# Performance work log

Hardware: AMD Instinct MI355X
Metric: run time of the kernel (lower is better)

The kernel has to match this reference:

```python
import jax, jax.numpy as jnp
import numpy as np

B, S, HID = 2, 2048, 2048
H, KVH, D = 32, 8, 64
G = H // KVH  # kv groups


def _rotate_half(x):
    x1, x2 = jnp.split(x, 2, axis=-1)
    return jnp.concatenate((-x2, x1), axis=-1)


def setup_inputs() -> dict:
    key = jax.random.key(0)
    ks = jax.random.split(key, 7)
    return {
        "hidden_states": jax.random.normal(ks[0], (B, S, HID), dtype=jnp.float32),
        "cos": jax.random.normal(ks[1], (B, S, D), dtype=jnp.float32),
        "sin": jax.random.normal(ks[2], (B, S, D), dtype=jnp.float32),
        "attention_mask": jnp.ones((B, S), dtype=bool),
        "Wq": jax.random.normal(ks[3], (HID, HID), dtype=jnp.float32) * 0.02,
        "Wk": jax.random.normal(ks[4], (KVH * D, HID), dtype=jnp.float32) * 0.02,
        "Wv": jax.random.normal(ks[5], (KVH * D, HID), dtype=jnp.float32) * 0.02,
        "Wo": jax.random.normal(ks[6], (HID, HID), dtype=jnp.float32) * 0.02,
    }


def reference(hidden_states, cos, sin, attention_mask, Wq, Wk, Wv, Wo):
    scaling = D ** (-0.5)
    # projections -> [B, heads, S, D]
    q = jnp.einsum('bsh,eh->bse', hidden_states, Wq).reshape(B, S, H, D).transpose(0, 2, 1, 3)
    k = jnp.einsum('bsh,eh->bse', hidden_states, Wk).reshape(B, S, KVH, D).transpose(0, 2, 1, 3)
    v = jnp.einsum('bsh,eh->bse', hidden_states, Wv).reshape(B, S, KVH, D).transpose(0, 2, 1, 3)
    # RoPE (cos/sin broadcast over head dim 1)
    c = cos[:, None, :, :]
    s = sin[:, None, :, :]
    q = q * c + _rotate_half(q) * s
    k = k * c + _rotate_half(k) * s
    # GQA: view q as [B, KVH, G, S, D]; avoid materializing expanded k/v
    qg = q.reshape(B, KVH, G, S, D)
    scores = jnp.einsum('bkgsd,bktd->bkgst', qg, k) * scaling  # [B,KVH,G,S,T]
    mask = attention_mask[:, None, None, None, :]  # [B,1,1,1,T]
    scores = jnp.where(mask, scores, -jnp.inf)
    attn = jax.nn.softmax(scores, axis=-1)
    out = jnp.einsum('bkgst,bktd->bkgsd', attn, v)  # [B,KVH,G,S,D]
    out = out.reshape(B, H, S, D).transpose(0, 2, 1, 3).reshape(B, S, H * D)
    return jnp.einsum('bse,he->bsh', out, Wo)
```

## Files before the change

kernel.cpp:

```cpp
#include <hip/hip_runtime.h>


typedef __attribute__((ext_vector_type(8))) short bf16x8;
typedef __attribute__((ext_vector_type(4))) float f32x4;

#define MFMA_BF16(a, b, c) __builtin_amdgcn_mfma_f32_16x16x32_bf16((a), (b), (c), 0, 0, 0)

#define QSCALE 0.1803368801111204f

static __device__ __forceinline__ unsigned short f2b(float f) {
  unsigned int u = __float_as_uint(f);
  return (unsigned short)((u + 0x7FFFu + ((u >> 16) & 1u)) >> 16);
}

typedef __attribute__((address_space(1))) void gvoid;
typedef __attribute__((address_space(3))) void svoid;
static __device__ __forceinline__ void gll16(const void* g, void* l) {
  __builtin_amdgcn_global_load_lds((gvoid*)g, (svoid*)l, 16, 0, 0);
}

typedef __attribute__((address_space(3))) unsigned short lds_us;
static __device__ __forceinline__ unsigned lof(unsigned short* p) {
  return (unsigned)(unsigned long long)(lds_us*)p;
}

template <int OFF>
static __device__ __forceinline__ bf16x8 dsr(unsigned a) {
  bf16x8 r;
  asm volatile("ds_read_b128 %0, %1 offset:%2" : "=v"(r) : "v"(a), "i"(OFF));
  return r;
}

template <int N>
static __device__ __forceinline__ void vm() {
  if constexpr (N >= 0) asm volatile("s_waitcnt vmcnt(%0)" ::"i"(N) : "memory");
}

#define BARRIER() asm volatile("s_barrier" ::: "memory")
#define LGKM0()                                        \
  do {                                                 \
    asm volatile("s_waitcnt lgkmcnt(0)" ::: "memory"); \
    __builtin_amdgcn_sched_barrier(0);                 \
  } while (0)

__global__ __launch_bounds__(256) void cvt4(
    const float* __restrict__ s0, const float* __restrict__ s1,
    const float* __restrict__ s2, const float* __restrict__ s3,
    unsigned short* __restrict__ d0, unsigned short* __restrict__ d1,
    unsigned short* __restrict__ d2, unsigned short* __restrict__ d3) {
  int i = blockIdx.x * 256 + threadIdx.x;
  const float* s; unsigned short* d; int off;
  if (i < 2097152)      { s = s0; d = d0; off = i; }
  else if (i < 3145728) { s = s1; d = d1; off = i - 2097152; }
  else if (i < 3407872) { s = s2; d = d2; off = i - 3145728; }
  else                  { s = s3; d = d3; off = i - 3407872; }
  float4 f = ((const float4*)s)[off];
  ushort4 o;
  o.x = f2b(f.x); o.y = f2b(f.y); o.z = f2b(f.z); o.w = f2b(f.w);
  ((ushort4*)d)[off] = o;
}

__global__ __launch_bounds__(256) void cvt_f32_bf16(const float* __restrict__ src,
                                                    unsigned short* __restrict__ dst,
                                                    int n4) {
  int i = blockIdx.x * 256 + threadIdx.x;
  if (i < n4) {
    float4 f = ((const float4*)src)[i];
    ushort4 o;
    o.x = f2b(f.x); o.y = f2b(f.y); o.z = f2b(f.z); o.w = f2b(f.w);
    ((ushort4*)dst)[i] = o;
  }
}


__global__ __launch_bounds__(512, 2) void gemm_qkv(
    const unsigned short* __restrict__ X,
    const unsigned short* __restrict__ W,
    const float* __restrict__ cosp,
    const float* __restrict__ sinp,
    unsigned short* __restrict__ Qo,
    unsigned short* __restrict__ Ko,
    unsigned short* __restrict__ Vto) {
  constexpr int K = 2048;
  __shared__ unsigned short As[2][16384];
  __shared__ unsigned short Bs[2][12288];

  const int tid = threadIdx.x;
  const int lane = tid & 63;
  const int w = tid >> 6;
  const int lane15 = lane & 15, quad = lane >> 4;
  const int l7 = lane15 & 7;

  const int id = blockIdx.x;
  const int wg = (id & 7) * 32 + (id >> 3);
  const int m0 = (wg >> 4) * 256;
  const int n0 = (wg & 15) * 192;

  f32x4 acc[2][12];
#pragma unroll
  for (int i = 0; i < 2; ++i)
#pragma unroll
    for (int j = 0; j < 12; ++j) acc[i][j] = (f32x4){0.f, 0.f, 0.f, 0.f};

  const int rl8 = lane >> 3;
  const int sc8 = ((lane & 7) ^ rl8) * 8;
  const unsigned short* Ab = X + (size_t)(m0 + w * 8 + rl8) * K + sc8;
  const unsigned short* Bb = W + (size_t)(n0 + w * 8 + rl8) * K + sc8;

  const unsigned As0b = lof(&As[0][0]);
  const unsigned Bs0b = lof(&Bs[0][0]);
  const int slot0 = (quad ^ l7) * 16;
  const int slot1 = ((4 | quad) ^ l7) * 16;
  const unsigned aA0 = As0b + (w * 32 + lane15) * 128 + slot0;
  const unsigned aA1 = As0b + (w * 32 + lane15) * 128 + slot1;
  const unsigned aB0 = Bs0b + lane15 * 128 + slot0;
  const unsigned aB1 = Bs0b + lane15 * 128 + slot1;

#define SB01_Q(bf, kk)                                      \
  do {                                                      \
    gll16(Bb + (kk), &Bs[bf][(w * 8) * 64]);                \
    gll16(Bb + 64 * K + (kk), &Bs[bf][(64 + w * 8) * 64]);  \
  } while (0)
#define SB2_Q(bf, kk) gll16(Bb + 128 * K + (kk), &Bs[bf][(128 + w * 8) * 64])
#define SA_Q(bf, kk)                                         \
  do {                                                       \
    gll16(Ab + (kk), &As[bf][(w * 8) * 64]);                 \
    gll16(Ab + 64 * K + (kk), &As[bf][(64 + w * 8) * 64]);   \
    gll16(Ab + 128 * K + (kk), &As[bf][(128 + w * 8) * 64]); \
    gll16(Ab + 192 * K + (kk), &As[bf][(192 + w * 8) * 64]); \
  } while (0)

#define DSRA_Q(CB, ks)                        \
  do {                                        \
    a[0] = dsr<(CB)*32768 + 0>(aA##ks);       \
    a[1] = dsr<(CB)*32768 + 2048>(aA##ks);    \
  } while (0)
#define DSRB_Q(CB, NH, ks)                                 \
  do {                                                     \
    bq[0] = dsr<(CB)*24576 + (NH)*12288 + 0>(aB##ks);      \
    bq[1] = dsr<(CB)*24576 + (NH)*12288 + 2048>(aB##ks);   \
    bq[2] = dsr<(CB)*24576 + (NH)*12288 + 4096>(aB##ks);   \
    bq[3] = dsr<(CB)*24576 + (NH)*12288 + 6144>(aB##ks);   \
    bq[4] = dsr<(CB)*24576 + (NH)*12288 + 8192>(aB##ks);   \
    bq[5] = dsr<(CB)*24576 + (NH)*12288 + 10240>(aB##ks);  \
  } while (0)
#define MM_Q(NH)                                                          \
  do {                                                                    \
    _Pragma("unroll") for (int mt = 0; mt < 2; ++mt)                      \
        _Pragma("unroll") for (int nf = 0; nf < 6; ++nf)                  \
            acc[mt][(NH)*6 + nf] =                                        \
                MFMA_BF16(a[mt], bq[nf], acc[mt][(NH)*6 + nf]);           \
  } while (0)

#define QTILE(CB, NB, KN, STG, VM0, VM3)                       \
  do {                                                         \
    bf16x8 a[2], bq[6];                                        \
                                              \
    DSRA_Q(CB, 0); DSRB_Q(CB, 0, 0);                           \
    if (STG) SB01_Q(NB, KN);                                   \
    vm<VM0>(); BARRIER(); LGKM0();                             \
    __builtin_amdgcn_s_setprio(1); MM_Q(0);                    \
    __builtin_amdgcn_s_setprio(0); BARRIER();                  \
                                   \
    DSRB_Q(CB, 1, 0);                                          \
    if (STG) { SA_Q(NB, KN); SB2_Q(NB, KN); }                  \
    BARRIER(); LGKM0();                                        \
    __builtin_amdgcn_s_setprio(1); MM_Q(1);                    \
    __builtin_amdgcn_s_setprio(0); BARRIER();                  \
                                              \
    DSRA_Q(CB, 1); DSRB_Q(CB, 0, 1);                           \
    BARRIER(); LGKM0();                                        \
    __builtin_amdgcn_s_setprio(1); MM_Q(0);                    \
    __builtin_amdgcn_s_setprio(0); BARRIER();                  \
                                              \
    DSRB_Q(CB, 1, 1);                                          \
    vm<VM3>(); BARRIER(); LGKM0();                             \
    __builtin_amdgcn_s_setprio(1); MM_Q(1);                    \
    __builtin_amdgcn_s_setprio(0); BARRIER();                  \
  } while (0)

  SB01_Q(0, 0);
  SA_Q(0, 0);
  SB2_Q(0, 0);
  vm<1>();
  BARRIER();

  for (int i = 0; i < 15; ++i) {
    const int kn0 = (2 * i + 1) * 64;
    const int kn1 = (2 * i + 2) * 64;
    QTILE(0, 1, kn0, 1, 2, 1);
    QTILE(1, 0, kn1, 1, 2, 1);
  }
  QTILE(0, 1, 31 * 64, 1, 2, 1);
  QTILE(1, 0, 0, 0, 0, -1);

#undef QTILE
#undef MM_Q
#undef DSRB_Q
#undef DSRA_Q
#undef SA_Q
#undef SB2_Q
#undef SB01_Q

#pragma unroll
  for (int mt = 0; mt < 2; ++mt) {
    const int mbase = m0 + w * 32 + mt * 16 + quad * 4;
#pragma unroll
    for (int nf = 0; nf < 12; ++nf) {
      const int n = n0 + nf * 16 + lane15;
      const int d = n & 63;
#pragma unroll
      for (int r = 0; r < 4; ++r) {
        const int mm = mbase + r;
        const int bb = mm >> 11;
        const int ss = mm & 2047;
        float v = acc[mt][nf][r];
        if (n < 2560) {
          const float partner = acc[mt][nf ^ 2][r];
          const float rot = ((d & 32) == 0) ? -partner : partner;
          v = v * cosp[(size_t)mm * 64 + d] + rot * sinp[(size_t)mm * 64 + d];
        }
        if (n < 2048) {
          const int hh = n >> 6;
          Qo[(((size_t)bb * 32 + hh) * 2048 + ss) * 64 + d] = f2b(v * QSCALE);
        } else if (n < 2560) {
          const int kvh = (n - 2048) >> 6;
          Ko[(((size_t)bb * 8 + kvh) * 2048 + ss) * 64 + d] = f2b(v);
        } else {
          const int kvh = (n - 2560) >> 6;
          Vto[(((size_t)bb * 8 + kvh) * 64 + d) * 2048 + ss] = f2b(v);
        }
      }
    }
  }
}

__global__ __launch_bounds__(512, 2) void gemm_out(
    const unsigned short* __restrict__ A,
    const unsigned short* __restrict__ W,
    float* __restrict__ out) {
  constexpr int K = 2048;
  __shared__ unsigned short As[2][16384];
  __shared__ unsigned short Bs[2][8192];

  const int tid = threadIdx.x;
  const int lane = tid & 63;
  const int w = tid >> 6;
  const int lane15 = lane & 15, quad = lane >> 4;
  const int l7 = lane15 & 7;
  const int wm = w >> 2, wn = w & 3;

  const int id = blockIdx.x;
  const int wg = (id & 7) * 32 + (id >> 3);
  const int m0 = (wg >> 4) * 256;
  const int n0 = (wg & 15) * 128;

  f32x4 acc[8][2];
#pragma unroll
  for (int i = 0; i < 8; ++i)
#pragma unroll
    for (int j = 0; j < 2; ++j) acc[i][j] = (f32x4){0.f, 0.f, 0.f, 0.f};

  const int rl8 = lane >> 3;
  const int sc8 = ((lane & 7) ^ rl8) * 8;
  const unsigned short* Ab = A + (size_t)(m0 + w * 8 + rl8) * K + sc8;
  const unsigned short* Bb = W + (size_t)(n0 + w * 8 + rl8) * K + sc8;

  const unsigned As0b = lof(&As[0][0]);
  const unsigned Bs0b = lof(&Bs[0][0]);
  const int slot0 = (quad ^ l7) * 16;
  const int slot1 = ((4 | quad) ^ l7) * 16;
  const unsigned aA0 = As0b + (wm * 128 + lane15) * 128 + slot0;
  const unsigned aA1 = As0b + (wm * 128 + lane15) * 128 + slot1;
  const unsigned aB0 = Bs0b + (wn * 32 + lane15) * 128 + slot0;
  const unsigned aB1 = Bs0b + (wn * 32 + lane15) * 128 + slot1;

#define SB_O(bf, kk)                                    \
  do {                                                  \
    gll16(Bb + (kk), &Bs[bf][(w * 8) * 64]);            \
    gll16(Bb + 64 * K + (kk), &Bs[bf][(64 + w * 8) * 64]); \
  } while (0)
#define SA_O(bf, kk)                                    \
  do {                                                  \
    gll16(Ab + (kk), &As[bf][(w * 8) * 64]);            \
    gll16(Ab + 128 * K + (kk), &As[bf][(128 + w * 8) * 64]); \
    gll16(Ab + 64 * K + (kk), &As[bf][(64 + w * 8) * 64]);   \
    gll16(Ab + 192 * K + (kk), &As[bf][(192 + w * 8) * 64]); \
  } while (0)

#define DSRA_O(CB, MH, ks)                                  \
  do {                                                      \
    a[0] = dsr<(CB)*32768 + (MH)*8192 + 0>(aA##ks);         \
    a[1] = dsr<(CB)*32768 + (MH)*8192 + 2048>(aA##ks);      \
    a[2] = dsr<(CB)*32768 + (MH)*8192 + 4096>(aA##ks);      \
    a[3] = dsr<(CB)*32768 + (MH)*8192 + 6144>(aA##ks);      \
  } while (0)
#define DSRB_O(CB, ks)                          \
  do {                                          \
    bq[0] = dsr<(CB)*16384 + 0>(aB##ks);        \
    bq[1] = dsr<(CB)*16384 + 2048>(aB##ks);     \
  } while (0)
#define MM_O(MB)                                                      \
  do {                                                                \
    _Pragma("unroll") for (int mf = 0; mf < 4; ++mf)                  \
        _Pragma("unroll") for (int nf = 0; nf < 2; ++nf)              \
            acc[(MB) + mf][nf] = MFMA_BF16(a[mf], bq[nf], acc[(MB) + mf][nf]); \
  } while (0)

#define OTILE(CB, NB, KN, STG, VM0, VM3)                       \
  do {                                                         \
    bf16x8 a[4], bq[2];                                        \
    DSRA_O(CB, 0, 0); DSRB_O(CB, 0);                           \
    if (STG) SB_O(NB, KN);                                     \
    vm<VM0>(); BARRIER(); LGKM0();                             \
    __builtin_amdgcn_s_setprio(1); MM_O(0);                    \
    __builtin_amdgcn_s_setprio(0); BARRIER();                  \
    DSRA_O(CB, 1, 0);                                          \
    if (STG) SA_O(NB, KN);                                     \
    BARRIER(); LGKM0();                                        \
    __builtin_amdgcn_s_setprio(1); MM_O(4);                    \
    __builtin_amdgcn_s_setprio(0); BARRIER();                  \
    DSRA_O(CB, 0, 1); DSRB_O(CB, 1);                           \
    BARRIER(); LGKM0();                                        \
    __builtin_amdgcn_s_setprio(1); MM_O(0);                    \
    __builtin_amdgcn_s_setprio(0); BARRIER();                  \
    DSRA_O(CB, 1, 1);                                          \
    vm<VM3>(); BARRIER(); LGKM0();                             \
    __builtin_amdgcn_s_setprio(1); MM_O(4);                    \
    __builtin_amdgcn_s_setprio(0); BARRIER();                  \
  } while (0)

  SB_O(0, 0);
  SA_O(0, 0);
  vm<2>();
  BARRIER();

  for (int i = 0; i < 15; ++i) {
    const int kn0 = (2 * i + 1) * 64;
    const int kn1 = (2 * i + 2) * 64;
    OTILE(0, 1, kn0, 1, 2, 2);
    OTILE(1, 0, kn1, 1, 2, 2);
  }
  OTILE(0, 1, 31 * 64, 1, 2, 2);
  OTILE(1, 0, 0, 0, 0, -1);

#undef OTILE
#undef MM_O
#undef DSRB_O
#undef DSRA_O
#undef SA_O
#undef SB_O

#pragma unroll
  for (int mf = 0; mf < 8; ++mf) {
    const int mbase = m0 + wm * 128 + mf * 16 + quad * 4;
#pragma unroll
    for (int nf = 0; nf < 2; ++nf) {
      const int n = n0 + wn * 32 + nf * 16 + lane15;
#pragma unroll
      for (int r = 0; r < 4; ++r)
        out[(size_t)(mbase + r) * 2048 + n] = acc[mf][nf][r];
    }
  }
}

__global__ __launch_bounds__(256) void attn(
    const unsigned short* __restrict__ Q,
    const unsigned short* __restrict__ Kg,
    const unsigned short* __restrict__ Vg,
    unsigned short* __restrict__ Ctx) {
  __shared__ unsigned short Ks[64 * 64];
  __shared__ unsigned short Vs[64 * 64];
  __shared__ unsigned short Ps[128 * 64];

  const int blk = blockIdx.x;
  const int qt = blk & 15;
  const int h = (blk >> 4) & 31;
  const int b = blk >> 9;
  const int kv = h >> 2;
  const int tid = threadIdx.x;
  const int lane = tid & 63;
  const int w = tid >> 6;
  const int lane15 = lane & 15, quad = lane >> 4;
  const int l7 = lane15 & 7;

  const short ONE = (short)0x3F80;
  const bf16x8 aone = (lane15 == 0)
      ? (bf16x8){ONE, ONE, ONE, ONE, ONE, ONE, ONE, ONE}
      : (bf16x8){0, 0, 0, 0, 0, 0, 0, 0};

  bf16x8 aq[2][2];
#pragma unroll
  for (int g = 0; g < 2; ++g) {
    const unsigned short* Qb =
        Q + (((size_t)b * 32 + h) * 2048 + qt * 128 + w * 32 + g * 16 + lane15) * 64;
    aq[g][0] = *(const bf16x8*)(Qb + quad * 8);
    aq[g][1] = *(const bf16x8*)(Qb + 32 + quad * 8);
  }

  const unsigned short* Kbase = Kg + ((size_t)b * 8 + kv) * 131072;
  const unsigned short* Vbase = Vg + ((size_t)b * 8 + kv) * 131072;

  f32x4 o[2][4], ol[2];
#pragma unroll
  for (int g = 0; g < 2; ++g) {
    ol[g] = (f32x4){0.f, 0.f, 0.f, 0.f};
#pragma unroll
    for (int mt = 0; mt < 4; ++mt) o[g][mt] = (f32x4){0.f, 0.f, 0.f, 0.f};
  }

  const int ur = tid >> 3;
  const int us = (tid & 7) * 8;
  const int sws = ur * 64 + 8 * ((tid & 7) ^ (ur & 7));

  uint4 kp0 = *(const uint4*)&Kbase[ur * 64 + us];
  uint4 kp1 = *(const uint4*)&Kbase[(ur + 32) * 64 + us];
  uint4 vp0 = *(const uint4*)&Vbase[(size_t)ur * 2048 + us];
  uint4 vp1 = *(const uint4*)&Vbase[(size_t)(ur + 32) * 2048 + us];

  const int prow0 = (w * 32 + lane15) * 64;
  const int prow1 = prow0 + 16 * 64;
  const int g0 = 8 * (quad ^ l7);

  for (int kt = 0; kt < 32; ++kt) {
    __syncthreads();
    *(uint4*)&Ks[sws] = kp0;
    *(uint4*)&Ks[sws + 32 * 64] = kp1;
    *(uint4*)&Vs[sws] = vp0;
    *(uint4*)&Vs[sws + 32 * 64] = vp1;
    const int kn = (kt + 1) & 31;
    kp0 = *(const uint4*)&Kbase[kn * 4096 + ur * 64 + us];
    kp1 = *(const uint4*)&Kbase[kn * 4096 + (ur + 32) * 64 + us];
    vp0 = *(const uint4*)&Vbase[(size_t)ur * 2048 + kn * 64 + us];
    vp1 = *(const uint4*)&Vbase[(size_t)(ur + 32) * 2048 + kn * 64 + us];
    __syncthreads();

#pragma unroll
    for (int nt = 0; nt < 4; ++nt) {
      const int krow = (nt * 16 + lane15) * 64;
      const bf16x8 k0f = *(const bf16x8*)&Ks[krow + g0];
      const bf16x8 k1f = *(const bf16x8*)&Ks[krow + (g0 ^ 32)];
#pragma unroll
      for (int g = 0; g < 2; ++g) {
        f32x4 c = (f32x4){0.f, 0.f, 0.f, 0.f};
        c = MFMA_BF16(k0f, aq[g][0], c);
        c = MFMA_BF16(k1f, aq[g][1], c);
        const unsigned u0 = __float_as_uint(__builtin_amdgcn_exp2f(c[0])) + 0x8000u;
        const unsigned u1 = __float_as_uint(__builtin_amdgcn_exp2f(c[1])) + 0x8000u;
        const unsigned u2 = __float_as_uint(__builtin_amdgcn_exp2f(c[2])) + 0x8000u;
        const unsigned u3 = __float_as_uint(__builtin_amdgcn_exp2f(c[3])) + 0x8000u;
        uint2 pk;
        pk.x = __builtin_amdgcn_perm(u1, u0, 0x07060302u);
        pk.y = __builtin_amdgcn_perm(u3, u2, 0x07060302u);
        const int pg = 8 * ((2 * nt + (quad >> 1)) ^ l7) + (quad & 1) * 4;
        *(uint2*)&Ps[(g ? prow1 : prow0) + pg] = pk;
      }
    }

#pragma unroll
    for (int f = 0; f < 2; ++f) {
      const bf16x8 bp0 = *(const bf16x8*)&Ps[prow0 + (g0 ^ (f * 32))];
      const bf16x8 bp1 = *(const bf16x8*)&Ps[prow1 + (g0 ^ (f * 32))];
      ol[0] = MFMA_BF16(aone, bp0, ol[0]);
      ol[1] = MFMA_BF16(aone, bp1, ol[1]);
#pragma unroll
      for (int mt = 0; mt < 4; ++mt) {
        const bf16x8 av = *(const bf16x8*)&Vs[(mt * 16 + lane15) * 64 + (g0 ^ (f * 32))];
        o[0][mt] = MFMA_BF16(av, bp0, o[0][mt]);
        o[1][mt] = MFMA_BF16(av, bp1, o[1][mt]);
      }
    }
  }

#pragma unroll
  for (int g = 0; g < 2; ++g) {
    const float ls = __shfl(ol[g][0], lane15, 64);
    const float inv = 1.f / ls;
    unsigned short* Cb =
        Ctx + ((size_t)b * 2048 + qt * 128 + w * 32 + g * 16 + lane15) * 2048 +
        h * 64 + quad * 4;
#pragma unroll
    for (int mt = 0; mt < 4; ++mt) {
      ushort4 st4;
      st4.x = f2b(o[g][mt][0] * inv);
      st4.y = f2b(o[g][mt][1] * inv);
      st4.z = f2b(o[g][mt][2] * inv);
      st4.w = f2b(o[g][mt][3] * inv);
      *(ushort4*)&Cb[mt * 16] = st4;
    }
  }
}

extern "C" void kernel_launch(void* const* d_in, const int* in_sizes, int n_in,
                              void* d_out, int out_size, void* d_ws, size_t ws_size,
                              hipStream_t stream) {
  const float* hs   = (const float*)d_in[0];
  const float* cosp = (const float*)d_in[1];
  const float* sinp = (const float*)d_in[2];
  const float* Wq = (const float*)d_in[4];
  const float* Wk = (const float*)d_in[5];
  const float* Wv = (const float*)d_in[6];
  const float* Wo = (const float*)d_in[7];
  float* out = (float*)d_out;
  unsigned short* ws = (unsigned short*)d_ws;

  unsigned short* Xbf  = ws;
  unsigned short* Ctx  = ws;
  unsigned short* Wqkv = ws + 8388608;
  unsigned short* Wob  = ws + 8388608;
  unsigned short* Qb   = ws + 14680064;
  unsigned short* Kb   = ws + 23068672;
  unsigned short* Vtb  = ws + 25165824;

  cvt4<<<14336, 256, 0, stream>>>(hs, Wq, Wk, Wv,
                                  Xbf, Wqkv, Wqkv + 4194304, Wqkv + 5242880);
  gemm_qkv<<<256, 512, 0, stream>>>(Xbf, Wqkv, cosp, sinp, Qb, Kb, Vtb);
  cvt_f32_bf16<<<4096, 256, 0, stream>>>(Wo, Wob, 1048576);
  attn<<<1024, 256, 0, stream>>>(Qb, Kb, Vtb, Ctx);
  gemm_out<<<256, 512, 0, stream>>>(Ctx, Wob, out);
}
```

Measured before the change: 328.6 us.

## Read K and V fragments directly from global memory instead of LDS staging

The attention kernel stops staging K and V tiles through shared memory with register prefetch and two block barriers per tile. Each wave now loads its MFMA K and V operand fragments straight from global memory, relying on the cache since all four waves read the same data. This removes the barriers and the LDS writes, but adds redundant global or L2 traffic per wave and exposes load latency with no explicit prefetch. The Ps buffer is still shared across the block.

```diff
diff --git a/kernel.cpp b/kernel.cpp
--- a/kernel.cpp
+++ b/kernel.cpp
@@ -369,8 +369,6 @@
     const unsigned short* __restrict__ Kg,
     const unsigned short* __restrict__ Vg,
     unsigned short* __restrict__ Ctx) {
-  __shared__ unsigned short Ks[64 * 64];
-  __shared__ unsigned short Vs[64 * 64];
   __shared__ unsigned short Ps[128 * 64];
 
   const int blk = blockIdx.x;
@@ -400,6 +398,8 @@
 
   const unsigned short* Kbase = Kg + ((size_t)b * 8 + kv) * 131072;
   const unsigned short* Vbase = Vg + ((size_t)b * 8 + kv) * 131072;
+  const unsigned short* Kl = Kbase + lane15 * 64 + quad * 8;
+  const unsigned short* Vl = Vbase + (size_t)lane15 * 2048 + quad * 8;
 
   f32x4 o[2][4], ol[2];
 #pragma unroll
@@ -408,38 +408,17 @@
 #pragma unroll
     for (int mt = 0; mt < 4; ++mt) o[g][mt] = (f32x4){0.f, 0.f, 0.f, 0.f};
   }
-
-  const int ur = tid >> 3;
-  const int us = (tid & 7) * 8;
-  const int sws = ur * 64 + 8 * ((tid & 7) ^ (ur & 7));
-
-  uint4 kp0 = *(const uint4*)&Kbase[ur * 64 + us];
-  uint4 kp1 = *(const uint4*)&Kbase[(ur + 32) * 64 + us];
-  uint4 vp0 = *(const uint4*)&Vbase[(size_t)ur * 2048 + us];
-  uint4 vp1 = *(const uint4*)&Vbase[(size_t)(ur + 32) * 2048 + us];
 
   const int prow0 = (w * 32 + lane15) * 64;
   const int prow1 = prow0 + 16 * 64;
   const int g0 = 8 * (quad ^ l7);
 
   for (int kt = 0; kt < 32; ++kt) {
-    __syncthreads();
-    *(uint4*)&Ks[sws] = kp0;
-    *(uint4*)&Ks[sws + 32 * 64] = kp1;
-    *(uint4*)&Vs[sws] = vp0;
-    *(uint4*)&Vs[sws + 32 * 64] = vp1;
-    const int kn = (kt + 1) & 31;
-    kp0 = *(const uint4*)&Kbase[kn * 4096 + ur * 64 + us];
-    kp1 = *(const uint4*)&Kbase[kn * 4096 + (ur + 32) * 64 + us];
-    vp0 = *(const uint4*)&Vbase[(size_t)ur * 2048 + kn * 64 + us];
-    vp1 = *(const uint4*)&Vbase[(size_t)(ur + 32) * 2048 + kn * 64 + us];
-    __syncthreads();
-
 #pragma unroll
     for (int nt = 0; nt < 4; ++nt) {
-      const int krow = (nt * 16 + lane15) * 64;
-      const bf16x8 k0f = *(const bf16x8*)&Ks[krow + g0];
-      const bf16x8 k1f = *(const bf16x8*)&Ks[krow + (g0 ^ 32)];
+      const unsigned short* kr = Kl + (kt * 64 + nt * 16) * 64;
+      const bf16x8 k0f = *(const bf16x8*)kr;
+      const bf16x8 k1f = *(const bf16x8*)(kr + 32);
 #pragma unroll
       for (int g = 0; g < 2; ++g) {
         f32x4 c = (f32x4){0.f, 0.f, 0.f, 0.f};
@@ -465,7 +444,8 @@
       ol[1] = MFMA_BF16(aone, bp1, ol[1]);
 #pragma unroll
       for (int mt = 0; mt < 4; ++mt) {
-        const bf16x8 av = *(const bf16x8*)&Vs[(mt * 16 + lane15) * 64 + (g0 ^ (f * 32))];
+        const bf16x8 av =
+            *(const bf16x8*)(Vl + (size_t)(mt * 16) * 2048 + kt * 64 + f * 32);
         o[0][mt] = MFMA_BF16(av, bp0, o[0][mt]);
         o[1][mt] = MFMA_BF16(av, bp1, o[1][mt]);
       }
```

Result: slower. 471.5 us (+43.5%).
